# Performance work log

Measured on AMD Instinct MI355X. Metric: run time of the kernel, lower is better.

Reference implementation:

```python
import jax, jax.numpy as jnp
import numpy as np

N, IN, OUT, T = 262144, 128, 128, 8

def setup_inputs() -> dict:
    key = jax.random.key(0)
    k1, k2, k3, k4 = jax.random.split(key, 4)
    x = jax.random.normal(k1, (N, IN), dtype=jnp.float32)
    x_type = jax.random.randint(k2, (N,), 0, T, dtype=jnp.int32)
    bound = 1.0 / np.sqrt(IN)
    # TypedLinear weight: [num_types, in_size, out_size]
    W = jax.random.uniform(k3, (T, IN, OUT), minval=-bound, maxval=bound, dtype=jnp.float32)
    b = jax.random.uniform(k4, (T, OUT), minval=-bound, maxval=bound, dtype=jnp.float32)
    return {"x": x, "x_type": x_type, "W": W, "b": b}

def reference(x, x_type, W, b):
    # Per-sample typed linear: out[n] = x[n] @ W[x_type[n]] + b[x_type[n]]
    # Grouped-GEMM formulation: loop over the small fixed set of types,
    # masking contributions, to avoid gathering a [N, IN, OUT] weight tensor.
    num_types = W.shape[0]
    out = jnp.zeros((x.shape[0], W.shape[2]), dtype=x.dtype)
    for t in range(num_types):
        mask = (x_type == t).astype(x.dtype)[:, None]  # [N,1]
        out = out + (x @ W[t]) * mask
    out = out + b[x_type]  # type-indexed bias gather
    return out
```

## Files before the change

### kernel.cpp

```cpp
#include <hip/hip_runtime.h>
#include <hip/hip_bf16.h>

#define N_ROWS 262144
#define IN_DIM 128
#define OUT_DIM 128
#define NTYPES 8
#define ROWS_PER_BLOCK 256
#define MAX_GROUPS 32

typedef short bf16x8 __attribute__((ext_vector_type(8)));
typedef float f32x4 __attribute__((ext_vector_type(4)));

__device__ __forceinline__ unsigned short f2bf_rne(float f) {
    unsigned int u = __float_as_uint(f);
    u += 0x7fff + ((u >> 16) & 1);
    return (unsigned short)(u >> 16);
}

__global__ void prep_w_kernel(const float* __restrict__ W, unsigned short* __restrict__ Wb) {
    __shared__ float tile[128 * 129];
    const int t = blockIdx.x;
    const float* Wt = W + t * (IN_DIM * OUT_DIM);
    for (int e = threadIdx.x; e < IN_DIM * OUT_DIM; e += blockDim.x) {
        int i = e >> 7;
        int o = e & 127;
        tile[i * 129 + o] = Wt[e];
    }
    __syncthreads();
    unsigned short* Wbt = Wb + t * (IN_DIM * OUT_DIM);
    for (int e = threadIdx.x; e < IN_DIM * OUT_DIM; e += blockDim.x) {
        int o = e >> 7;
        int i = e & 127;
        Wbt[e] = f2bf_rne(tile[i * 129 + o]);
    }
}

__global__ void __launch_bounds__(256) typed_linear_kernel(
        const float* __restrict__ x, const int* __restrict__ xt,
        const unsigned short* __restrict__ Wb, const float* __restrict__ bias,
        float* __restrict__ out) {
    __shared__ int s_cnt[NTYPES];
    __shared__ int s_cursor[NTYPES];
    __shared__ unsigned short s_list[ROWS_PER_BLOCK];
    __shared__ unsigned char s_gtype[MAX_GROUPS];
    __shared__ short s_gstart[MAX_GROUPS];
    __shared__ unsigned char s_gcnt[MAX_GROUPS];
    __shared__ int s_ngroups;

    const int tid = threadIdx.x;
    const int row0 = blockIdx.x * ROWS_PER_BLOCK;

    if (tid < NTYPES) s_cnt[tid] = 0;
    __syncthreads();
    const int my_t = xt[row0 + tid];
    atomicAdd(&s_cnt[my_t], 1);
    __syncthreads();
    if (tid == 0) {
        int acc = 0, g = 0;
        for (int i = 0; i < NTYPES; ++i) {
            int c = s_cnt[i];
            s_cursor[i] = acc;
            for (int s = 0; s < c; s += 16) {
                s_gtype[g] = (unsigned char)i;
                s_gstart[g] = (short)(acc + s);
                s_gcnt[g] = (unsigned char)((c - s) < 16 ? (c - s) : 16);
                ++g;
            }
            acc += c;
        }
        s_ngroups = g;
    }
    __syncthreads();
    {
        int pos = atomicAdd(&s_cursor[my_t], 1);
        s_list[pos] = (unsigned short)tid;
    }
    __syncthreads();

    const int wave = tid >> 6;
    const int lane = tid & 63;
    const int m = lane & 15;
    const int q = lane >> 4;
    const int ngroups = s_ngroups;

    for (int g = wave; g < ngroups; g += 4) {
        const int t  = s_gtype[g];
        const int gs = s_gstart[g];
        const int gc = s_gcnt[g];

        const int mm = (m < gc) ? m : (gc - 1);
        const int arow = row0 + s_list[gs + mm];
        const float* xr = x + (size_t)arow * IN_DIM + q * 8;
        bf16x8 afrag[4];
        #pragma unroll
        for (int kc = 0; kc < 4; ++kc) {
            const float4 f0 = *reinterpret_cast<const float4*>(xr + kc * 32);
            const float4 f1 = *reinterpret_cast<const float4*>(xr + kc * 32 + 4);
            union { bf16x8 v; __hip_bfloat162 h[4]; } u;
            u.h[0] = __float22bfloat162_rn(make_float2(f0.x, f0.y));
            u.h[1] = __float22bfloat162_rn(make_float2(f0.z, f0.w));
            u.h[2] = __float22bfloat162_rn(make_float2(f1.x, f1.y));
            u.h[3] = __float22bfloat162_rn(make_float2(f1.z, f1.w));
            afrag[kc] = u.v;
        }

        int orow[4];
        #pragma unroll
        for (int r = 0; r < 4; ++r) {
            const int mr = q * 4 + r;
            orow[r] = (mr < gc) ? (row0 + s_list[gs + mr]) : -1;
        }

        const unsigned short* wt = Wb + t * (IN_DIM * OUT_DIM);
        const float* bt = bias + t * OUT_DIM;
        #pragma unroll
        for (int nt = 0; nt < 8; ++nt) {
            f32x4 acc = {0.f, 0.f, 0.f, 0.f};
            const unsigned short* wcol = wt + (nt * 16 + m) * IN_DIM + q * 8;
            #pragma unroll
            for (int kc = 0; kc < 4; ++kc) {
                const bf16x8 bfrag = *reinterpret_cast<const bf16x8*>(wcol + kc * 32);
                acc = __builtin_amdgcn_mfma_f32_16x16x32_bf16(afrag[kc], bfrag, acc, 0, 0, 0);
            }
            const float bv = bt[nt * 16 + m];
            #pragma unroll
            for (int r = 0; r < 4; ++r) {
                if (orow[r] >= 0) {
                    out[(size_t)orow[r] * OUT_DIM + nt * 16 + m] = acc[r] + bv;
                }
            }
        }
    }
}

extern "C" void kernel_launch(void* const* d_in, const int* in_sizes, int n_in,
                              void* d_out, int out_size, void* d_ws, size_t ws_size,
                              hipStream_t stream) {
    const float* x  = (const float*)d_in[0];
    const int* xt   = (const int*)d_in[1];
    const float* W  = (const float*)d_in[2];
    const float* b  = (const float*)d_in[3];
    float* out      = (float*)d_out;
    unsigned short* Wb = (unsigned short*)d_ws;

    prep_w_kernel<<<NTYPES, 256, 0, stream>>>(W, Wb);
    typed_linear_kernel<<<N_ROWS / ROWS_PER_BLOCK, 256, 0, stream>>>(x, xt, Wb, b, out);
}
```

Measured before the change: 340.3 us.

## Process 32-row type groups per wave and split weight prep across more blocks

Each wave now handles a group of up to 32 same-type rows as two 16-row MFMA sub-tiles. Those sub-tiles share the bf16 weight fragments, which are loaded four output tiles at a time, so each weight load feeds twice as many MFMAs. The weight transpose/convert prep kernel is split into 32 blocks, each with a 32-row shared tile instead of one 128x129 tile per block, to spread that work across more CUs. The cost is more registers per wave (A fragments for two sub-tiles plus 16 B fragments), which may lower occupancy. Larger groups also mean fewer groups per block, so wave load balance can worsen when type counts are uneven.

```diff
diff --git a/kernel.cpp b/kernel.cpp
--- a/kernel.cpp
+++ b/kernel.cpp
@@ -6,7 +6,8 @@
 #define OUT_DIM 128
 #define NTYPES 8
 #define ROWS_PER_BLOCK 256
-#define MAX_GROUPS 32
+#define GROUP_M 32
+#define MAX_GROUPS 16
 
 typedef short bf16x8 __attribute__((ext_vector_type(8)));
 typedef float f32x4 __attribute__((ext_vector_type(4)));
@@ -18,20 +19,21 @@
 }
 
 __global__ void prep_w_kernel(const float* __restrict__ W, unsigned short* __restrict__ Wb) {
-    __shared__ float tile[128 * 129];
-    const int t = blockIdx.x;
+    __shared__ float tile[32 * 129];
+    const int t = blockIdx.x >> 2;
+    const int i0 = (blockIdx.x & 3) * 32;
     const float* Wt = W + t * (IN_DIM * OUT_DIM);
-    for (int e = threadIdx.x; e < IN_DIM * OUT_DIM; e += blockDim.x) {
+    for (int e = threadIdx.x; e < 32 * 128; e += blockDim.x) {
         int i = e >> 7;
         int o = e & 127;
-        tile[i * 129 + o] = Wt[e];
+        tile[i * 129 + o] = Wt[(i0 + i) * OUT_DIM + o];
     }
     __syncthreads();
     unsigned short* Wbt = Wb + t * (IN_DIM * OUT_DIM);
-    for (int e = threadIdx.x; e < IN_DIM * OUT_DIM; e += blockDim.x) {
-        int o = e >> 7;
-        int i = e & 127;
-        Wbt[e] = f2bf_rne(tile[i * 129 + o]);
+    for (int e = threadIdx.x; e < 32 * 128; e += blockDim.x) {
+        int o = e >> 5;
+        int i = e & 31;
+        Wbt[o * IN_DIM + i0 + i] = f2bf_rne(tile[i * 129 + o]);
     }
 }
 
@@ -60,10 +62,10 @@
         for (int i = 0; i < NTYPES; ++i) {
             int c = s_cnt[i];
             s_cursor[i] = acc;
-            for (int s = 0; s < c; s += 16) {
+            for (int s = 0; s < c; s += GROUP_M) {
                 s_gtype[g] = (unsigned char)i;
                 s_gstart[g] = (short)(acc + s);
-                s_gcnt[g] = (unsigned char)((c - s) < 16 ? (c - s) : 16);
+                s_gcnt[g] = (unsigned char)((c - s) < GROUP_M ? (c - s) : GROUP_M);
                 ++g;
             }
             acc += c;
@@ -88,45 +90,65 @@
         const int gs = s_gstart[g];
         const int gc = s_gcnt[g];
 
-        const int mm = (m < gc) ? m : (gc - 1);
-        const int arow = row0 + s_list[gs + mm];
-        const float* xr = x + (size_t)arow * IN_DIM + q * 8;
-        bf16x8 afrag[4];
+        bf16x8 afrag[2][4];
         #pragma unroll
-        for (int kc = 0; kc < 4; ++kc) {
-            const float4 f0 = *reinterpret_cast<const float4*>(xr + kc * 32);
-            const float4 f1 = *reinterpret_cast<const float4*>(xr + kc * 32 + 4);
-            union { bf16x8 v; __hip_bfloat162 h[4]; } u;
-            u.h[0] = __float22bfloat162_rn(make_float2(f0.x, f0.y));
-            u.h[1] = __float22bfloat162_rn(make_float2(f0.z, f0.w));
-            u.h[2] = __float22bfloat162_rn(make_float2(f1.x, f1.y));
-            u.h[3] = __float22bfloat162_rn(make_float2(f1.z, f1.w));
-            afrag[kc] = u.v;
+        for (int sub = 0; sub < 2; ++sub) {
+            const int mrow = sub * 16 + m;
+            const int mm = (mrow < gc) ? mrow : (gc - 1);
+            const float* xr = x + (size_t)(row0 + s_list[gs + mm]) * IN_DIM + q * 8;
+            #pragma unroll
+            for (int kc = 0; kc < 4; ++kc) {
+                const float4 f0 = *reinterpret_cast<const float4*>(xr + kc * 32);
+                const float4 f1 = *reinterpret_cast<const float4*>(xr + kc * 32 + 4);
+                union { bf16x8 v; __hip_bfloat162 h[4]; } u;
+                u.h[0] = __float22bfloat162_rn(make_float2(f0.x, f0.y));
+                u.h[1] = __float22bfloat162_rn(make_float2(f0.z, f0.w));
+                u.h[2] = __float22bfloat162_rn(make_float2(f1.x, f1.y));
+                u.h[3] = __float22bfloat162_rn(make_float2(f1.z, f1.w));
+                afrag[sub][kc] = u.v;
+            }
         }
 
-        int orow[4];
+        int orow[2][4];
         #pragma unroll
-        for (int r = 0; r < 4; ++r) {
-            const int mr = q * 4 + r;
-            orow[r] = (mr < gc) ? (row0 + s_list[gs + mr]) : -1;
-        }
+        for (int sub = 0; sub < 2; ++sub)
+            #pragma unroll
+            for (int r = 0; r < 4; ++r) {
+                const int mr = sub * 16 + q * 4 + r;
+                orow[sub][r] = (mr < gc) ? (row0 + s_list[gs + mr]) : -1;
+            }
 
         const unsigned short* wt = Wb + t * (IN_DIM * OUT_DIM);
         const float* bt = bias + t * OUT_DIM;
+
         #pragma unroll
-        for (int nt = 0; nt < 8; ++nt) {
-            f32x4 acc = {0.f, 0.f, 0.f, 0.f};
-            const unsigned short* wcol = wt + (nt * 16 + m) * IN_DIM + q * 8;
+        for (int half = 0; half < 2; ++half) {
+            bf16x8 bfrag[4][4];
             #pragma unroll
-            for (int kc = 0; kc < 4; ++kc) {
-                const bf16x8 bfrag = *reinterpret_cast<const bf16x8*>(wcol + kc * 32);
-                acc = __builtin_amdgcn_mfma_f32_16x16x32_bf16(afrag[kc], bfrag, acc, 0, 0, 0);
+            for (int nt2 = 0; nt2 < 4; ++nt2) {
+                const int nt = half * 4 + nt2;
+                const unsigned short* wcol = wt + (nt * 16 + m) * IN_DIM + q * 8;
+                #pragma unroll
+                for (int kc = 0; kc < 4; ++kc)
+                    bfrag[nt2][kc] = *reinterpret_cast<const bf16x8*>(wcol + kc * 32);
             }
-            const float bv = bt[nt * 16 + m];
             #pragma unroll
-            for (int r = 0; r < 4; ++r) {
-                if (orow[r] >= 0) {
-                    out[(size_t)orow[r] * OUT_DIM + nt * 16 + m] = acc[r] + bv;
+            for (int nt2 = 0; nt2 < 4; ++nt2) {
+                const int nt = half * 4 + nt2;
+                f32x4 acc0 = {0.f, 0.f, 0.f, 0.f};
+                f32x4 acc1 = {0.f, 0.f, 0.f, 0.f};
+                #pragma unroll
+                for (int kc = 0; kc < 4; ++kc) {
+                    acc0 = __builtin_amdgcn_mfma_f32_16x16x32_bf16(afrag[0][kc], bfrag[nt2][kc], acc0, 0, 0, 0);
+                    acc1 = __builtin_amdgcn_mfma_f32_16x16x32_bf16(afrag[1][kc], bfrag[nt2][kc], acc1, 0, 0, 0);
+                }
+                const float bv = bt[nt * 16 + m];
+                #pragma unroll
+                for (int r = 0; r < 4; ++r) {
+                    if (orow[0][r] >= 0)
+                        out[(size_t)orow[0][r] * OUT_DIM + nt * 16 + m] = acc0[r] + bv;
+                    if (orow[1][r] >= 0)
+                        out[(size_t)orow[1][r] * OUT_DIM + nt * 16 + m] = acc1[r] + bv;
                 }
             }
         }
@@ -143,6 +165,6 @@
     float* out      = (float*)d_out;
     unsigned short* Wb = (unsigned short*)d_ws;
 
-    prep_w_kernel<<<NTYPES, 256, 0, stream>>>(W, Wb);
+    prep_w_kernel<<<NTYPES * 4, 256, 0, stream>>>(W, Wb);
     typed_linear_kernel<<<N_ROWS / ROWS_PER_BLOCK, 256, 0, stream>>>(x, xt, Wb, b, out);
 }
```

Measured after the change: 319.4 us. -6.1%, faster.

## Stage x rows via async global-to-LDS copies and batch weight fragment loads

Applied to the files above, without the earlier changes.

Gathered x rows are now loaded with global_load_lds async copies into a per-wave XOR-swizzled LDS staging buffer, then read back to build bf16 A fragments. This replaces the strided per-lane global float4 reads. Weight fragments for two N-tiles are loaded before their MFMAs so more loads are in flight. The weight prep kernel is split across 1024 small blocks instead of 8, which parallelises the transpose-and-convert at the cost of uncoalesced reads. The 32KB of added LDS and the launch-bounds hint may limit occupancy.

```diff
diff --git a/kernel.cpp b/kernel.cpp
--- a/kernel.cpp
+++ b/kernel.cpp
@@ -6,6 +6,7 @@
 #define OUT_DIM 128
 #define NTYPES 8
 #define ROWS_PER_BLOCK 256
+#define GROUP_M 16
 #define MAX_GROUPS 32
 
 typedef short bf16x8 __attribute__((ext_vector_type(8)));
@@ -17,28 +18,26 @@
     return (unsigned short)(u >> 16);
 }
 
-__global__ void prep_w_kernel(const float* __restrict__ W, unsigned short* __restrict__ Wb) {
-    __shared__ float tile[128 * 129];
-    const int t = blockIdx.x;
-    const float* Wt = W + t * (IN_DIM * OUT_DIM);
-    for (int e = threadIdx.x; e < IN_DIM * OUT_DIM; e += blockDim.x) {
-        int i = e >> 7;
-        int o = e & 127;
-        tile[i * 129 + o] = Wt[e];
-    }
-    __syncthreads();
-    unsigned short* Wbt = Wb + t * (IN_DIM * OUT_DIM);
-    for (int e = threadIdx.x; e < IN_DIM * OUT_DIM; e += blockDim.x) {
-        int o = e >> 7;
-        int i = e & 127;
-        Wbt[e] = f2bf_rne(tile[i * 129 + o]);
-    }
+__device__ __forceinline__ void async_copy16(const float* g, float* lds_base) {
+    __builtin_amdgcn_global_load_lds(
+        (const __attribute__((address_space(1))) void*)g,
+        (__attribute__((address_space(3))) void*)lds_base,
+        16, 0, 0);
 }
 
-__global__ void __launch_bounds__(256) typed_linear_kernel(
+__global__ void __launch_bounds__(128) prep_w_kernel(const float* __restrict__ W,
+                                                     unsigned short* __restrict__ Wb) {
+    const int t = blockIdx.x >> 7;
+    const int o = blockIdx.x & 127;
+    const int i = threadIdx.x;
+    Wb[(t * OUT_DIM + o) * IN_DIM + i] = f2bf_rne(W[(t * IN_DIM + i) * OUT_DIM + o]);
+}
+
+__global__ void __launch_bounds__(256, 4) typed_linear_kernel(
         const float* __restrict__ x, const int* __restrict__ xt,
         const unsigned short* __restrict__ Wb, const float* __restrict__ bias,
         float* __restrict__ out) {
+    __shared__ float s_stage[4][2048];
     __shared__ int s_cnt[NTYPES];
     __shared__ int s_cursor[NTYPES];
     __shared__ unsigned short s_list[ROWS_PER_BLOCK];
@@ -60,10 +59,10 @@
         for (int i = 0; i < NTYPES; ++i) {
             int c = s_cnt[i];
             s_cursor[i] = acc;
-            for (int s = 0; s < c; s += 16) {
+            for (int s = 0; s < c; s += GROUP_M) {
                 s_gtype[g] = (unsigned char)i;
                 s_gstart[g] = (short)(acc + s);
-                s_gcnt[g] = (unsigned char)((c - s) < 16 ? (c - s) : 16);
+                s_gcnt[g] = (unsigned char)((c - s) < GROUP_M ? (c - s) : GROUP_M);
                 ++g;
             }
             acc += c;
@@ -81,27 +80,23 @@
     const int lane = tid & 63;
     const int m = lane & 15;
     const int q = lane >> 4;
+    const int l5 = lane >> 5;
+    const int c_lo = lane & 31;
     const int ngroups = s_ngroups;
+    float* stage = s_stage[wave];
 
     for (int g = wave; g < ngroups; g += 4) {
         const int t  = s_gtype[g];
         const int gs = s_gstart[g];
         const int gc = s_gcnt[g];
 
-        const int mm = (m < gc) ? m : (gc - 1);
-        const int arow = row0 + s_list[gs + mm];
-        const float* xr = x + (size_t)arow * IN_DIM + q * 8;
-        bf16x8 afrag[4];
         #pragma unroll
-        for (int kc = 0; kc < 4; ++kc) {
-            const float4 f0 = *reinterpret_cast<const float4*>(xr + kc * 32);
-            const float4 f1 = *reinterpret_cast<const float4*>(xr + kc * 32 + 4);
-            union { bf16x8 v; __hip_bfloat162 h[4]; } u;
-            u.h[0] = __float22bfloat162_rn(make_float2(f0.x, f0.y));
-            u.h[1] = __float22bfloat162_rn(make_float2(f0.z, f0.w));
-            u.h[2] = __float22bfloat162_rn(make_float2(f1.x, f1.y));
-            u.h[3] = __float22bfloat162_rn(make_float2(f1.z, f1.w));
-            afrag[kc] = u.v;
+        for (int j = 0; j < 8; ++j) {
+            const int mrow = j * 2 + l5;
+            const int mm = (mrow < gc) ? mrow : (gc - 1);
+            const int row = row0 + s_list[gs + mm];
+            const int c = c_lo ^ mrow;
+            async_copy16(x + (size_t)row * IN_DIM + c * 4, stage + j * 256);
         }
 
         int orow[4];
@@ -113,20 +108,46 @@
 
         const unsigned short* wt = Wb + t * (IN_DIM * OUT_DIM);
         const float* bt = bias + t * OUT_DIM;
+
+        asm volatile("s_waitcnt vmcnt(0)" ::: "memory");
+
+        bf16x8 afrag[4];
         #pragma unroll
-        for (int nt = 0; nt < 8; ++nt) {
-            f32x4 acc = {0.f, 0.f, 0.f, 0.f};
-            const unsigned short* wcol = wt + (nt * 16 + m) * IN_DIM + q * 8;
+        for (int kc = 0; kc < 4; ++kc) {
+            const int c0 = kc * 8 + q * 2;
+            const float4 f0 = *reinterpret_cast<const float4*>(stage + (m * 32 + (c0 ^ m)) * 4);
+            const float4 f1 = *reinterpret_cast<const float4*>(stage + (m * 32 + ((c0 + 1) ^ m)) * 4);
+            union { bf16x8 v; __hip_bfloat162 h[4]; } u;
+            u.h[0] = __float22bfloat162_rn(make_float2(f0.x, f0.y));
+            u.h[1] = __float22bfloat162_rn(make_float2(f0.z, f0.w));
+            u.h[2] = __float22bfloat162_rn(make_float2(f1.x, f1.y));
+            u.h[3] = __float22bfloat162_rn(make_float2(f1.z, f1.w));
+            afrag[kc] = u.v;
+        }
+
+        #pragma unroll
+        for (int h = 0; h < 4; ++h) {
+            bf16x8 bfrag[2][4];
             #pragma unroll
-            for (int kc = 0; kc < 4; ++kc) {
-                const bf16x8 bfrag = *reinterpret_cast<const bf16x8*>(wcol + kc * 32);
-                acc = __builtin_amdgcn_mfma_f32_16x16x32_bf16(afrag[kc], bfrag, acc, 0, 0, 0);
+            for (int nn = 0; nn < 2; ++nn) {
+                const int nt = h * 2 + nn;
+                const unsigned short* wcol = wt + (nt * 16 + m) * IN_DIM + q * 8;
+                #pragma unroll
+                for (int kc = 0; kc < 4; ++kc)
+                    bfrag[nn][kc] = *reinterpret_cast<const bf16x8*>(wcol + kc * 32);
             }
-            const float bv = bt[nt * 16 + m];
             #pragma unroll
-            for (int r = 0; r < 4; ++r) {
-                if (orow[r] >= 0) {
-                    out[(size_t)orow[r] * OUT_DIM + nt * 16 + m] = acc[r] + bv;
+            for (int nn = 0; nn < 2; ++nn) {
+                const int nt = h * 2 + nn;
+                f32x4 acc = {0.f, 0.f, 0.f, 0.f};
+                #pragma unroll
+                for (int kc = 0; kc < 4; ++kc)
+                    acc = __builtin_amdgcn_mfma_f32_16x16x32_bf16(afrag[kc], bfrag[nn][kc], acc, 0, 0, 0);
+                const float bv = bt[nt * 16 + m];
+                #pragma unroll
+                for (int r = 0; r < 4; ++r) {
+                    if (orow[r] >= 0)
+                        out[(size_t)orow[r] * OUT_DIM + nt * 16 + m] = acc[r] + bv;
                 }
             }
         }
@@ -143,6 +164,6 @@
     float* out      = (float*)d_out;
     unsigned short* Wb = (unsigned short*)d_ws;
 
-    prep_w_kernel<<<NTYPES, 256, 0, stream>>>(W, Wb);
+    prep_w_kernel<<<NTYPES * OUT_DIM, 128, 0, stream>>>(W, Wb);
     typed_linear_kernel<<<N_ROWS / ROWS_PER_BLOCK, 256, 0, stream>>>(x, xt, Wb, b, out);
 }
```

Measured after the change: 308.1 us. 1.1x faster.
